# Optimization experiments

Measured on AMD Instinct MI355X. Metric: run time of the kernel, lower is better.

Reference implementation:

```python
import jax, jax.numpy as jnp
import numpy as np

IN_FEATURES = 4096
OUT_FEATURES = 4096
SHARED_ROWS = 256
BATCH = 8192


def setup_inputs() -> dict:
    key = jax.random.key(0)
    k_x, k_w, k_b = jax.random.split(key, 3)
    x = jax.random.normal(k_x, (BATCH, IN_FEATURES), dtype=jnp.float32)
    shared_weights = jax.random.normal(k_w, (SHARED_ROWS, IN_FEATURES), dtype=jnp.float32)
    bias = jax.random.normal(k_b, (OUT_FEATURES,), dtype=jnp.float32)
    return {"x": x, "shared_weights": shared_weights, "bias": bias}


def reference(x, shared_weights, bias):
    # Faithful to torch: weight_matrix = shared_weights.repeat(out//shared, 1)
    reps = OUT_FEATURES // SHARED_ROWS
    weight_matrix = jnp.tile(shared_weights, (reps, 1))  # [out_features, in_features]
    # y = x @ W^T + b  -> [batch, out_features]
    return jnp.matmul(x, weight_matrix.T) + bias
```

## Files before the change

### kernel.cpp

```cpp
#include <hip/hip_runtime.h>
#include <cstdint>
#include <cstddef>

#define M_DIM 8192
#define N_DIM 256
#define K_DIM 4096
#define OUT_F 4096
#define BM 32
#define BN 128
#define BK 64
#define NTH 512

typedef float    float4_  __attribute__((ext_vector_type(4)));
typedef _Float16 half8    __attribute__((ext_vector_type(8)));
typedef _Float16 half4    __attribute__((ext_vector_type(4)));

__global__ __launch_bounds__(256) void convert_w_kernel(const float* __restrict__ w,
                                                        _Float16* __restrict__ wh) {
  int i = (blockIdx.x * 256 + threadIdx.x) * 8;
  float4_ f0 = *(const float4_*)(w + i);
  float4_ f1 = *(const float4_*)(w + i + 4);
  half8 h;
  h[0] = (_Float16)f0[0]; h[1] = (_Float16)f0[1];
  h[2] = (_Float16)f0[2]; h[3] = (_Float16)f0[3];
  h[4] = (_Float16)f1[0]; h[5] = (_Float16)f1[1];
  h[6] = (_Float16)f1[2]; h[7] = (_Float16)f1[3];
  *(half8*)(wh + i) = h;
}

__device__ __forceinline__ void load_bfrag(half8 b[2], const _Float16* __restrict__ wg,
                                           int kk) {
  b[0] = *(const half8*)(wg + kk);
  b[1] = *(const half8*)(wg + kk + 32);
}

__device__ __forceinline__ void stage_a(_Float16* __restrict__ As, int arow, int asw,
                                        float4_ a) {
  half4 h;
  h[0] = (_Float16)a[0]; h[1] = (_Float16)a[1];
  h[2] = (_Float16)a[2]; h[3] = (_Float16)a[3];
  *(half4*)(As + arow * BK + asw) = h;
}

__device__ __forceinline__ void mfma_step(float4_ acc[2], const half8 b[2],
                                          const _Float16* __restrict__ As,
                                          int l16, int quad) {
#pragma unroll
  for (int ks = 0; ks < 2; ++ks) {
    const int off = ((ks * 4 + quad) ^ (l16 & 7)) << 3;
    half8 a0 = *(const half8*)(As + l16 * BK + off);
    half8 a1 = *(const half8*)(As + (16 + l16) * BK + off);
    acc[0] = __builtin_amdgcn_mfma_f32_16x16x32_f16(a0, b[ks], acc[0], 0, 0, 0);
    acc[1] = __builtin_amdgcn_mfma_f32_16x16x32_f16(a1, b[ks], acc[1], 0, 0, 0);
  }
}

__global__ __launch_bounds__(NTH, 4) void fused_kernel(const float* __restrict__ x,
                                                       const _Float16* __restrict__ wh,
                                                       const float* __restrict__ bias,
                                                       float* __restrict__ out) {
  __shared__ __align__(16) _Float16 As[2][BM * BK];
  __shared__ __align__(16) float Ssh[BM][BN + 4];
  __shared__ __align__(16) float bsh[16 * BN];

  const int tid  = threadIdx.x;
  const int wv   = tid >> 6;
  const int lane = tid & 63;
  const int quad = lane >> 4;
  const int l16  = lane & 15;
  const int m0   = blockIdx.x * BM;
  const int nb   = blockIdx.y * BN;

  {
    const float4_* b4 = (const float4_*)bias;
    float4_* bs4 = (float4_*)bsh;
    bs4[tid] = b4[(tid >> 5) * (N_DIM / 4) + (nb >> 2) + (tid & 31)];
  }

  const int arow = tid >> 4;
  const int ac4  = tid & 15;
  const int asw  = ((((ac4 >> 1) ^ (arow & 7)) << 3) | ((ac4 & 1) << 2));
  const float* xg = x + (size_t)(m0 + arow) * K_DIM + ac4 * 4;

  const _Float16* wg = wh + (size_t)(nb + wv * 16 + l16) * K_DIM + quad * 8;

  float4_ acc[2];
  acc[0] = (float4_){0.f, 0.f, 0.f, 0.f};
  acc[1] = (float4_){0.f, 0.f, 0.f, 0.f};

  half8 bA[2], bB[2];
  float4_ aP0 = *(const float4_*)(xg);
  float4_ aP1 = *(const float4_*)(xg + BK);
  load_bfrag(bA, wg, 0);
  stage_a(As[0], arow, asw, aP0);
  aP0 = *(const float4_*)(xg + 2 * BK);
  __syncthreads();

  const int NKT = K_DIM / BK;
  for (int kt = 0; kt < NKT; kt += 2) {
    load_bfrag(bB, wg, (kt + 1) * BK);
    stage_a(As[1], arow, asw, aP1);
    if (kt + 3 < NKT) aP1 = *(const float4_*)(xg + (kt + 3) * BK);
    mfma_step(acc, bA, As[0], l16, quad);
    __syncthreads();

    if (kt + 2 < NKT) {
      load_bfrag(bA, wg, (kt + 2) * BK);
      stage_a(As[0], arow, asw, aP0);
      if (kt + 4 < NKT) aP0 = *(const float4_*)(xg + (kt + 4) * BK);
    }
    mfma_step(acc, bB, As[1], l16, quad);
    __syncthreads();
  }

#pragma unroll
  for (int mf = 0; mf < 2; ++mf)
#pragma unroll
    for (int r = 0; r < 4; ++r)
      Ssh[mf * 16 + quad * 4 + r][wv * 16 + l16] = acc[mf][r];
  __syncthreads();

  float4_* out4 = (float4_*)out;
  const float4_* bs4 = (const float4_*)bsh;
#pragma unroll
  for (int p = 0; p < 2; ++p) {
    const int row = wv * 4 + p * 2 + (lane >> 5);
    const int c4  = lane & 31;
    float4_ sv = *(const float4_*)(&Ssh[row][c4 * 4]);
    const size_t obase = (size_t)(m0 + row) * (OUT_F / 4) + (nb >> 2);
#pragma unroll
    for (int rep = 0; rep < 16; ++rep)
      __builtin_nontemporal_store(sv + bs4[rep * (BN / 4) + c4],
                                  out4 + obase + rep * (N_DIM / 4) + c4);
  }
}

extern "C" void kernel_launch(void* const* d_in, const int* in_sizes, int n_in,
                              void* d_out, int out_size, void* d_ws, size_t ws_size,
                              hipStream_t stream) {
  const float* x    = (const float*)d_in[0];
  const float* w    = (const float*)d_in[1];
  const float* bias = (const float*)d_in[2];
  float* out        = (float*)d_out;
  _Float16* wh      = (_Float16*)d_ws;

  convert_w_kernel<<<(N_DIM * K_DIM) / (256 * 8), 256, 0, stream>>>(w, wh);
  fused_kernel<<<dim3(M_DIM / BM, 2), NTH, 0, stream>>>(x, wh, bias, out);
}
```

Baseline: 270.6 us.

## Switch to 32x32x16 MFMA with 4 waves per block and phase barriers

Replaces the 8-wave block using 16x16x32 MFMAs with a 4-wave block in which each wave computes a 32x32 output tile using the 32x32x16 f16 MFMA. A-tile staging now converts 8 floats per thread into one half8 store, and the loop uses explicit sched_barrier/s_barrier phases and s_setprio around the MFMA groups. Epilogue indexing and the bias load are adjusted to the new accumulator layout. The aim is fewer instructions per FLOP and less LDS traffic per MFMA, at the cost of fewer waves per block and lower occupancy (launch bounds go from 4 to 2), which may hide memory latency less well in this memory-bound GEMM.

```diff
diff --git a/kernel.cpp b/kernel.cpp
--- a/kernel.cpp
+++ b/kernel.cpp
@@ -9,11 +9,12 @@
 #define BM 32
 #define BN 128
 #define BK 64
-#define NTH 512
+#define NTH 256
+#define NKT (K_DIM / BK)
 
-typedef float    float4_  __attribute__((ext_vector_type(4)));
-typedef _Float16 half8    __attribute__((ext_vector_type(8)));
-typedef _Float16 half4    __attribute__((ext_vector_type(4)));
+typedef float    float4_ __attribute__((ext_vector_type(4)));
+typedef float    f32x16  __attribute__((ext_vector_type(16)));
+typedef _Float16 half8   __attribute__((ext_vector_type(8)));
 
 __global__ __launch_bounds__(256) void convert_w_kernel(const float* __restrict__ w,
                                                         _Float16* __restrict__ wh) {
@@ -28,34 +29,24 @@
   *(half8*)(wh + i) = h;
 }
 
-__device__ __forceinline__ void load_bfrag(half8 b[2], const _Float16* __restrict__ wg,
-                                           int kk) {
-  b[0] = *(const half8*)(wg + kk);
-  b[1] = *(const half8*)(wg + kk + 32);
+__device__ __forceinline__ void stage_a(_Float16* __restrict__ dst,
+                                        float4_ x0, float4_ x1) {
+  half8 h;
+  h[0] = (_Float16)x0[0]; h[1] = (_Float16)x0[1];
+  h[2] = (_Float16)x0[2]; h[3] = (_Float16)x0[3];
+  h[4] = (_Float16)x1[0]; h[5] = (_Float16)x1[1];
+  h[6] = (_Float16)x1[2]; h[7] = (_Float16)x1[3];
+  *(half8*)dst = h;
 }
 
-__device__ __forceinline__ void stage_a(_Float16* __restrict__ As, int arow, int asw,
-                                        float4_ a) {
-  half4 h;
-  h[0] = (_Float16)a[0]; h[1] = (_Float16)a[1];
-  h[2] = (_Float16)a[2]; h[3] = (_Float16)a[3];
-  *(half4*)(As + arow * BK + asw) = h;
-}
+#define PHASE_BARRIER() do {                              \
+    __builtin_amdgcn_sched_barrier(0);                    \
+    asm volatile("s_waitcnt lgkmcnt(0)" ::: "memory");    \
+    __builtin_amdgcn_s_barrier();                         \
+    __builtin_amdgcn_sched_barrier(0);                    \
+  } while (0)
 
-__device__ __forceinline__ void mfma_step(float4_ acc[2], const half8 b[2],
-                                          const _Float16* __restrict__ As,
-                                          int l16, int quad) {
-#pragma unroll
-  for (int ks = 0; ks < 2; ++ks) {
-    const int off = ((ks * 4 + quad) ^ (l16 & 7)) << 3;
-    half8 a0 = *(const half8*)(As + l16 * BK + off);
-    half8 a1 = *(const half8*)(As + (16 + l16) * BK + off);
-    acc[0] = __builtin_amdgcn_mfma_f32_16x16x32_f16(a0, b[ks], acc[0], 0, 0, 0);
-    acc[1] = __builtin_amdgcn_mfma_f32_16x16x32_f16(a1, b[ks], acc[1], 0, 0, 0);
-  }
-}
-
-__global__ __launch_bounds__(NTH, 4) void fused_kernel(const float* __restrict__ x,
+__global__ __launch_bounds__(NTH, 2) void fused_kernel(const float* __restrict__ x,
                                                        const _Float16* __restrict__ wh,
                                                        const float* __restrict__ bias,
                                                        float* __restrict__ out) {
@@ -66,72 +57,114 @@
   const int tid  = threadIdx.x;
   const int wv   = tid >> 6;
   const int lane = tid & 63;
-  const int quad = lane >> 4;
-  const int l16  = lane & 15;
+  const int l32  = lane & 31;
+  const int hk   = lane >> 5;
   const int m0   = blockIdx.x * BM;
   const int nb   = blockIdx.y * BN;
 
   {
     const float4_* b4 = (const float4_*)bias;
     float4_* bs4 = (float4_*)bsh;
-    bs4[tid] = b4[(tid >> 5) * (N_DIM / 4) + (nb >> 2) + (tid & 31)];
+#pragma unroll
+    for (int p = 0; p < 2; ++p) {
+      int idx = p * NTH + tid;
+      int rep = idx >> 5, c4 = idx & 31;
+      bs4[idx] = b4[rep * (N_DIM / 4) + (nb >> 2) + c4];
+    }
   }
 
-  const int arow = tid >> 4;
-  const int ac4  = tid & 15;
-  const int asw  = ((((ac4 >> 1) ^ (arow & 7)) << 3) | ((ac4 & 1) << 2));
-  const float* xg = x + (size_t)(m0 + arow) * K_DIM + ac4 * 4;
+  const int arow = tid >> 3;
+  const int ag   = tid & 7;
+  const float* xg = x + (size_t)(m0 + arow) * K_DIM + ag * 8;
+  _Float16* awr = &As[0][0] + arow * BK + ((ag ^ (arow & 7)) << 3);
 
-  const _Float16* wg = wh + (size_t)(nb + wv * 16 + l16) * K_DIM + quad * 8;
+  const _Float16* ard = &As[0][0] + l32 * BK;
+  const int aoff0 = (((0 * 2 + hk) ^ (l32 & 7)) << 3);
+  const int aoff1 = (((1 * 2 + hk) ^ (l32 & 7)) << 3);
+  const int aoff2 = (((2 * 2 + hk) ^ (l32 & 7)) << 3);
+  const int aoff3 = (((3 * 2 + hk) ^ (l32 & 7)) << 3);
 
-  float4_ acc[2];
-  acc[0] = (float4_){0.f, 0.f, 0.f, 0.f};
-  acc[1] = (float4_){0.f, 0.f, 0.f, 0.f};
+  const _Float16* wg = wh + (size_t)(nb + wv * 32 + l32) * K_DIM + hk * 8;
 
-  half8 bA[2], bB[2];
-  float4_ aP0 = *(const float4_*)(xg);
-  float4_ aP1 = *(const float4_*)(xg + BK);
-  load_bfrag(bA, wg, 0);
-  stage_a(As[0], arow, asw, aP0);
-  aP0 = *(const float4_*)(xg + 2 * BK);
-  __syncthreads();
+  f32x16 acc = {};
 
-  const int NKT = K_DIM / BK;
+  float4_ t00 = *(const float4_*)(xg);
+  float4_ t01 = *(const float4_*)(xg + 4);
+  float4_ xE0 = *(const float4_*)(xg + BK);
+  float4_ xE1 = *(const float4_*)(xg + BK + 4);
+  float4_ xO0 = *(const float4_*)(xg + 2 * BK);
+  float4_ xO1 = *(const float4_*)(xg + 2 * BK + 4);
+  half8 bfA[4], bfB[4];
+#pragma unroll
+  for (int ks = 0; ks < 4; ++ks) bfA[ks] = *(const half8*)(wg + ks * 16);
+  stage_a(awr, t00, t01);
+  PHASE_BARRIER();
+
   for (int kt = 0; kt < NKT; kt += 2) {
-    load_bfrag(bB, wg, (kt + 1) * BK);
-    stage_a(As[1], arow, asw, aP1);
-    if (kt + 3 < NKT) aP1 = *(const float4_*)(xg + (kt + 3) * BK);
-    mfma_step(acc, bA, As[0], l16, quad);
-    __syncthreads();
-
-    if (kt + 2 < NKT) {
-      load_bfrag(bA, wg, (kt + 2) * BK);
-      stage_a(As[0], arow, asw, aP0);
-      if (kt + 4 < NKT) aP0 = *(const float4_*)(xg + (kt + 4) * BK);
+    {
+      stage_a(awr + BM * BK, xE0, xE1);
+      const int t3 = (kt + 3 < NKT ? kt + 3 : NKT - 1) * BK;
+      xE0 = *(const float4_*)(xg + t3);
+      xE1 = *(const float4_*)(xg + t3 + 4);
+#pragma unroll
+      for (int ks = 0; ks < 4; ++ks)
+        bfB[ks] = *(const half8*)(wg + (kt + 1) * BK + ks * 16);
+      half8 a0 = *(const half8*)(ard + aoff0);
+      half8 a1 = *(const half8*)(ard + aoff1);
+      half8 a2 = *(const half8*)(ard + aoff2);
+      half8 a3 = *(const half8*)(ard + aoff3);
+      __builtin_amdgcn_s_setprio(1);
+      acc = __builtin_amdgcn_mfma_f32_32x32x16_f16(a0, bfA[0], acc, 0, 0, 0);
+      acc = __builtin_amdgcn_mfma_f32_32x32x16_f16(a1, bfA[1], acc, 0, 0, 0);
+      acc = __builtin_amdgcn_mfma_f32_32x32x16_f16(a2, bfA[2], acc, 0, 0, 0);
+      acc = __builtin_amdgcn_mfma_f32_32x32x16_f16(a3, bfA[3], acc, 0, 0, 0);
+      __builtin_amdgcn_s_setprio(0);
+      PHASE_BARRIER();
     }
-    mfma_step(acc, bB, As[1], l16, quad);
-    __syncthreads();
+    {
+      if (kt + 2 < NKT) stage_a(awr, xO0, xO1);
+      const int t4 = (kt + 4 < NKT ? kt + 4 : NKT - 1) * BK;
+      xO0 = *(const float4_*)(xg + t4);
+      xO1 = *(const float4_*)(xg + t4 + 4);
+      const int tB = (kt + 2 < NKT ? kt + 2 : NKT - 1) * BK;
+#pragma unroll
+      for (int ks = 0; ks < 4; ++ks)
+        bfA[ks] = *(const half8*)(wg + tB + ks * 16);
+      const _Float16* rd = ard + BM * BK;
+      half8 a0 = *(const half8*)(rd + aoff0);
+      half8 a1 = *(const half8*)(rd + aoff1);
+      half8 a2 = *(const half8*)(rd + aoff2);
+      half8 a3 = *(const half8*)(rd + aoff3);
+      __builtin_amdgcn_s_setprio(1);
+      acc = __builtin_amdgcn_mfma_f32_32x32x16_f16(a0, bfB[0], acc, 0, 0, 0);
+      acc = __builtin_amdgcn_mfma_f32_32x32x16_f16(a1, bfB[1], acc, 0, 0, 0);
+      acc = __builtin_amdgcn_mfma_f32_32x32x16_f16(a2, bfB[2], acc, 0, 0, 0);
+      acc = __builtin_amdgcn_mfma_f32_32x32x16_f16(a3, bfB[3], acc, 0, 0, 0);
+      __builtin_amdgcn_s_setprio(0);
+      PHASE_BARRIER();
+    }
   }
 
 #pragma unroll
-  for (int mf = 0; mf < 2; ++mf)
-#pragma unroll
-    for (int r = 0; r < 4; ++r)
-      Ssh[mf * 16 + quad * 4 + r][wv * 16 + l16] = acc[mf][r];
+  for (int r = 0; r < 16; ++r) {
+    const int m = (r & 3) + 8 * (r >> 2) + 4 * hk;
+    Ssh[m][wv * 32 + l32] = acc[r];
+  }
   __syncthreads();
 
-  float4_* out4 = (float4_*)out;
   const float4_* bs4 = (const float4_*)bsh;
+  const int c4 = l32;
 #pragma unroll
-  for (int p = 0; p < 2; ++p) {
-    const int row = wv * 4 + p * 2 + (lane >> 5);
-    const int c4  = lane & 31;
+  for (int ri = 0; ri < 8; ++ri) {
+    const int row = wv * 8 + ri;
     float4_ sv = *(const float4_*)(&Ssh[row][c4 * 4]);
-    const size_t obase = (size_t)(m0 + row) * (OUT_F / 4) + (nb >> 2);
+    float* orow = out + (size_t)(m0 + row) * OUT_F + nb;
 #pragma unroll
-    for (int rep = 0; rep < 16; ++rep)
-      __builtin_nontemporal_store(sv + bs4[rep * (BN / 4) + c4],
-                                  out4 + obase + rep * (N_DIM / 4) + c4);
+    for (int rr = 0; rr < 8; ++rr) {
+      const int rep = rr * 2 + hk;
+      float4_ bv = bs4[rep * (BN / 4) + c4];
+      __builtin_nontemporal_store(sv + bv, (float4_*)(orow + rep * N_DIM) + c4);
+    }
   }
 }
 
```

Result: slower. 284.1 us (+5.0%).
